# Optimization experiments

Measured on AMD Instinct MI355X. Metric: run time of the kernel, lower is better.

Reference implementation:

```python
import jax, jax.numpy as jnp
import numpy as np

NBINS = (128, 64, 32)
N_POINTS = 250_000
N_GENES = 5000
N_GENES_OI = 500
SUM_H = sum(NBINS)            # 224
SUM_W = sum(n - 1 for n in NBINS)  # 221


def _calculate_widths(unnormalized_widths):
    return jax.nn.softmax(unnormalized_widths, axis=-1)


def _calculate_bin_locations(widths):
    bl = jnp.cumsum(widths, axis=-1)
    bl = bl.at[..., -1].set(1.0)
    pad = [(0, 0)] * (bl.ndim - 1) + [(1, 0)]
    return jnp.pad(bl, pad)


def _calculate_heights(unnormalized_heights, widths):
    e = jnp.exp(unnormalized_heights)
    # trapezoid-rule area so pdf integrates to 1
    area = jnp.sum(0.5 * (e[..., :-1] + e[..., 1:]) * widths, axis=-1, keepdims=True)
    return e / area


def _calculate_bin_left_cdf(heights, widths):
    cdf = jnp.cumsum(0.5 * (heights[..., :-1] + heights[..., 1:]) * widths, axis=-1)
    cdf = cdf.at[..., -1].set(1.0)
    pad = [(0, 0)] * (cdf.ndim - 1) + [(1, 0)]
    return jnp.pad(cdf, pad)


def _quadratic_spline(x, widths, heights, bin_left_cdf, bin_locations):
    # all per-point: widths [N,nb], heights [N,nb+1], cdf/locations [N,nb+1]
    nb = widths.shape[-1]
    bin_idx = jnp.clip(jnp.sum(x[:, None] >= bin_locations, axis=-1) - 1, 0, nb - 1)

    def take(a, i):
        return jnp.take_along_axis(a, i[:, None], axis=-1)[:, 0]

    in_bl = take(bin_locations, bin_idx)
    in_cdf = take(bin_left_cdf, bin_idx)
    h_left = take(heights, bin_idx)
    h_right = take(heights, bin_idx + 1)
    w = take(widths, bin_idx)

    a = 0.5 * (h_right - h_left) * w
    b = h_left * w
    alpha = (x - in_bl) / w
    out = a * alpha * alpha + b * alpha + in_cdf
    logabsdet = jnp.log(alpha * (h_right - h_left) + h_left)
    return jnp.clip(out, 0.0, 1.0), logabsdet


def setup_inputs() -> dict:
    key = jax.random.key(0)
    k1, k2, k3, k4, k5, k6 = jax.random.split(key, 6)
    return {
        "x": jax.random.uniform(k1, (N_POINTS,), dtype=jnp.float32),
        "delta": jax.random.normal(k2, (N_POINTS, SUM_H), dtype=jnp.float32),
        "heights_weight": jax.random.normal(k3, (N_GENES, SUM_H), dtype=jnp.float32),
        "widths_weight": jax.random.normal(k4, (N_GENES, SUM_W), dtype=jnp.float32),
        "genes_oi": jax.random.randint(k5, (N_GENES_OI,), 0, N_GENES, dtype=jnp.int32),
        "local_gene_ix": jax.random.randint(k6, (N_POINTS,), 0, N_GENES_OI, dtype=jnp.int32),
    }


def reference(x, delta, heights_weight, widths_weight, genes_oi, local_gene_ix):
    # sparse embedding gather for the genes in the minibatch
    uh_all = heights_weight[genes_oi]   # [G_oi, sum_h]
    uw_all = widths_weight[genes_oi]    # [G_oi, sum_w]

    outputs = x
    logabsdet = jnp.zeros_like(x)
    h_off = 0
    w_off = 0
    d_off = 0
    for n in NBINS:
        uw = uw_all[:, w_off:w_off + (n - 1)]          # [G_oi, n-1]
        uh = uh_all[:, h_off:h_off + n]                # [G_oi, n]
        dh = delta[:, d_off:d_off + n]                 # [N, n]

        widths_g = _calculate_widths(uw)               # [G_oi, n-1]
        bin_loc_g = _calculate_bin_locations(widths_g) # [G_oi, n]

        widths = widths_g[local_gene_ix]               # [N, n-1]
        bin_locations = bin_loc_g[local_gene_ix]       # [N, n]
        uh_p = uh[local_gene_ix] + dh                  # [N, n]
        heights = _calculate_heights(uh_p, widths)     # [N, n]
        bin_left_cdf = _calculate_bin_left_cdf(heights, widths)  # [N, n]

        outputs, lad = _quadratic_spline(outputs, widths, heights, bin_left_cdf, bin_locations)
        logabsdet = logabsdet + lad

        h_off += n
        w_off += n - 1
        d_off += n
    return outputs, logabsdet
```

## Files before the change

kernel.cpp:

```cpp
#include <hip/hip_runtime.h>
#include <math.h>

#define SUM_H 224
#define SUM_W 221
#define ROWP  224

__global__ __launch_bounds__(64) void gene_tables_kernel(
    const float* __restrict__ heights_weight,
    const float* __restrict__ widths_weight,
    const int*   __restrict__ genes_oi,
    float* __restrict__ uh_t,
    float* __restrict__ w_t,
    float* __restrict__ bl_t,
    int n_genes)
{
    int g = blockIdx.x;
    if (g >= n_genes) return;
    int gi = genes_oi[g];
    int l  = threadIdx.x;

    {
        const float* src = heights_weight + (size_t)gi * SUM_H;
        float*       dst = uh_t + (size_t)g * ROWP;
        for (int j = l; j < SUM_H; j += 64) dst[j] = src[j];
    }

    const float* wsrc  = widths_weight + (size_t)gi * SUM_W;
    float*       wdst  = w_t  + (size_t)g * ROWP;
    float*       bldst = bl_t + (size_t)g * ROWP;

    const int ns[3]   = {128, 64, 32};
    const int woff[3] = {0, 127, 190};
    const int toff[3] = {0, 128, 192};

    for (int lev = 0; lev < 3; lev++) {
        int m  = ns[lev] - 1;
        int j0 = 2 * l, j1 = 2 * l + 1;
        float u0 = (j0 < m) ? wsrc[woff[lev] + j0] : -1e30f;
        float u1 = (j1 < m) ? wsrc[woff[lev] + j1] : -1e30f;
        float mx = fmaxf(u0, u1);
        #pragma unroll
        for (int msk = 32; msk >= 1; msk >>= 1)
            mx = fmaxf(mx, __shfl_xor(mx, msk, 64));
        float e0 = (j0 < m) ? __expf(u0 - mx) : 0.f;
        float e1 = (j1 < m) ? __expf(u1 - mx) : 0.f;
        float local = e0 + e1;
        float incl  = local;
        #pragma unroll
        for (int off = 1; off < 64; off <<= 1) {
            float t = __shfl_up(incl, off, 64);
            if (l >= off) incl += t;
        }
        float total = __shfl(incl, 63, 64);
        float inv   = 1.0f / total;
        float excl  = incl - local;
        if (j0 < m) wdst[toff[lev] + j0] = e0 * inv;
        if (j1 < m) wdst[toff[lev] + j1] = e1 * inv;
        float c0 = (excl + e0) * inv;
        float c1 = (excl + e0 + e1) * inv;
        if (j0 <= m - 2) bldst[toff[lev] + j0 + 1] = c0;
        if (j1 <= m - 2) bldst[toff[lev] + j1 + 1] = c1;
        if (l == 0) {
            bldst[toff[lev]]     = 0.0f;
            bldst[toff[lev] + m] = 1.0f;
        }
    }
}

template<int N>
__device__ inline void level_step(
    const float* __restrict__ dh,
    const float* __restrict__ uh,
    const float* __restrict__ bl,
    const float* __restrict__ wt,
    int e, float& x, float& lad)
{
    constexpr int NCH = (N + 63) / 64;
    constexpr int ACT = (N >= 64) ? 16 : (N / 4);

    float s[NCH][4];
    int cnt = 0;
    #pragma unroll
    for (int ch = 0; ch < NCH; ch++) {
        int c = ch * 64 + 4 * e;
        bool act = (e < ACT);
        if (act) {
            float4 dh4 = *reinterpret_cast<const float4*>(dh + c);
            float4 uh4 = *reinterpret_cast<const float4*>(uh + c);
            float4 bl4 = *reinterpret_cast<const float4*>(bl + c);
            float4 w4  = *reinterpret_cast<const float4*>(wt + c);
            bool hx = (c + 4) <= (N - 1);
            float dhx = hx ? dh[c + 4] : 0.f;
            float uhx = hx ? uh[c + 4] : 0.f;
            float E0 = __expf(uh4.x + dh4.x);
            float E1 = __expf(uh4.y + dh4.y);
            float E2 = __expf(uh4.z + dh4.z);
            float E3 = __expf(uh4.w + dh4.w);
            float E4 = __expf(uhx + dhx);
            cnt += (x >= bl4.x) + (x >= bl4.y) + (x >= bl4.z) + (x >= bl4.w);
            s[ch][0] = 0.5f * (E0 + E1) * w4.x;
            s[ch][1] = 0.5f * (E1 + E2) * w4.y;
            s[ch][2] = 0.5f * (E2 + E3) * w4.z;
            s[ch][3] = ((c + 3) <= (N - 2)) ? 0.5f * (E3 + E4) * w4.w : 0.f;
        } else {
            s[ch][0] = s[ch][1] = s[ch][2] = s[ch][3] = 0.f;
        }
    }

    #pragma unroll
    for (int msk = 8; msk >= 1; msk >>= 1)
        cnt += __shfl_xor(cnt, msk, 16);
    int idx = cnt - 1;
    if (idx > N - 2) idx = N - 2;

    float area = 0.f, part = 0.f;
    #pragma unroll
    for (int ch = 0; ch < NCH; ch++) {
        int c = ch * 64 + 4 * e;
        #pragma unroll
        for (int k = 0; k < 4; k++) {
            area += s[ch][k];
            part += ((c + k) < idx) ? s[ch][k] : 0.f;
        }
    }
    #pragma unroll
    for (int msk = 8; msk >= 1; msk >>= 1) {
        area += __shfl_xor(area, msk, 16);
        part += __shfl_xor(part, msk, 16);
    }

    float in_bl = bl[idx];
    float w     = wt[idx];
    float El    = __expf(uh[idx]     + dh[idx]);
    float Er    = __expf(uh[idx + 1] + dh[idx + 1]);

    float inv   = 1.0f / area;
    float hl    = El * inv;
    float hr    = Er * inv;
    float icdf  = part * inv;
    float alpha = (x - in_bl) / w;
    float dhh   = hr - hl;
    float out   = (0.5f * dhh * w) * alpha * alpha + (hl * w) * alpha + icdf;
    lad += __logf(alpha * dhh + hl);
    x = fminf(fmaxf(out, 0.f), 1.f);
}

__global__ __launch_bounds__(256) void spline_kernel(
    const float* __restrict__ x_in,
    const float* __restrict__ delta,
    const int*   __restrict__ lgx,
    const float* __restrict__ uh_t,
    const float* __restrict__ w_t,
    const float* __restrict__ bl_t,
    float* __restrict__ out,
    float* __restrict__ lad_out,
    int n_points)
{
    int tid = blockIdx.x * blockDim.x + threadIdx.x;
    int p = tid >> 4;
    int e = tid & 15;
    if (p >= n_points) return;

    int   g   = lgx[p];
    float x   = x_in[p];
    float lad = 0.f;

    const float* dh = delta + (size_t)p * SUM_H;
    const float* uh = uh_t + (size_t)g * ROWP;
    const float* bl = bl_t + (size_t)g * ROWP;
    const float* wt = w_t  + (size_t)g * ROWP;

    level_step<128>(dh,       uh,       bl,       wt,       e, x, lad);
    level_step<64> (dh + 128, uh + 128, bl + 128, wt + 128, e, x, lad);
    level_step<32> (dh + 192, uh + 192, bl + 192, wt + 192, e, x, lad);

    if (e == 0) {
        out[p]     = x;
        lad_out[p] = lad;
    }
}

extern "C" void kernel_launch(void* const* d_in, const int* in_sizes, int n_in,
                              void* d_out, int out_size, void* d_ws, size_t ws_size,
                              hipStream_t stream)
{
    const float* x        = (const float*)d_in[0];
    const float* delta    = (const float*)d_in[1];
    const float* hw       = (const float*)d_in[2];
    const float* ww       = (const float*)d_in[3];
    const int*   genes_oi = (const int*)  d_in[4];
    const int*   lgx      = (const int*)  d_in[5];

    int n_points   = in_sizes[0];
    int n_genes_oi = in_sizes[4];

    float* uh_t = (float*)d_ws;
    float* w_t  = uh_t + (size_t)n_genes_oi * ROWP;
    float* bl_t = w_t  + (size_t)n_genes_oi * ROWP;

    hipLaunchKernelGGL(gene_tables_kernel, dim3(n_genes_oi), dim3(64), 0, stream,
                       hw, ww, genes_oi, uh_t, w_t, bl_t, n_genes_oi);

    const int threads = 256;
    const int ppb     = threads / 16;
    const int blocks  = (n_points + ppb - 1) / ppb;
    hipLaunchKernelGGL(spline_kernel, dim3(blocks), dim3(threads), 0, stream,
                       x, delta, lgx, uh_t, w_t, bl_t,
                       (float*)d_out, (float*)d_out + n_points, n_points);
}
```

Baseline: 377.5 us.

## Prefetch all three spline levels into registers and select bins via shuffles

The spline kernel now loads the delta, height, bin-location and half-width data for all three levels at the start. Exps and areas are computed from registers, and each level's bin is selected with a register select followed by a shuffle from the owning lane, replacing the dependent global reloads that followed the bin search. Height weights are read straight from the gene table through genes_oi, which removes the copy in the table kernel. The 0.5 factor is folded into the stored widths and the trailing entries are zero-padded. This exposes more memory parallelism and removes serialized loads, at the cost of higher register pressure.

```diff
diff --git a/kernel.cpp b/kernel.cpp
--- a/kernel.cpp
+++ b/kernel.cpp
@@ -6,11 +6,9 @@
 #define ROWP  224
 
 __global__ __launch_bounds__(64) void gene_tables_kernel(
-    const float* __restrict__ heights_weight,
     const float* __restrict__ widths_weight,
     const int*   __restrict__ genes_oi,
-    float* __restrict__ uh_t,
-    float* __restrict__ w_t,
+    float* __restrict__ wh_t,
     float* __restrict__ bl_t,
     int n_genes)
 {
@@ -19,14 +17,8 @@
     int gi = genes_oi[g];
     int l  = threadIdx.x;
 
-    {
-        const float* src = heights_weight + (size_t)gi * SUM_H;
-        float*       dst = uh_t + (size_t)g * ROWP;
-        for (int j = l; j < SUM_H; j += 64) dst[j] = src[j];
-    }
-
     const float* wsrc  = widths_weight + (size_t)gi * SUM_W;
-    float*       wdst  = w_t  + (size_t)g * ROWP;
+    float*       wdst  = wh_t + (size_t)g * ROWP;
     float*       bldst = bl_t + (size_t)g * ROWP;
 
     const int ns[3]   = {128, 64, 32};
@@ -54,8 +46,8 @@
         float total = __shfl(incl, 63, 64);
         float inv   = 1.0f / total;
         float excl  = incl - local;
-        if (j0 < m) wdst[toff[lev] + j0] = e0 * inv;
-        if (j1 < m) wdst[toff[lev] + j1] = e1 * inv;
+        if (j0 < m) wdst[toff[lev] + j0] = 0.5f * e0 * inv;
+        if (j1 < m) wdst[toff[lev] + j1] = 0.5f * e1 * inv;
         float c0 = (excl + e0) * inv;
         float c1 = (excl + e0 + e1) * inv;
         if (j0 <= m - 2) bldst[toff[lev] + j0 + 1] = c0;
@@ -65,92 +57,120 @@
             bldst[toff[lev] + m] = 1.0f;
         }
     }
-}
-
-template<int N>
-__device__ inline void level_step(
-    const float* __restrict__ dh,
-    const float* __restrict__ uh,
-    const float* __restrict__ bl,
-    const float* __restrict__ wt,
-    int e, float& x, float& lad)
-{
-    constexpr int NCH = (N + 63) / 64;
-    constexpr int ACT = (N >= 64) ? 16 : (N / 4);
-
-    float s[NCH][4];
-    int cnt = 0;
-    #pragma unroll
-    for (int ch = 0; ch < NCH; ch++) {
-        int c = ch * 64 + 4 * e;
-        bool act = (e < ACT);
-        if (act) {
-            float4 dh4 = *reinterpret_cast<const float4*>(dh + c);
-            float4 uh4 = *reinterpret_cast<const float4*>(uh + c);
-            float4 bl4 = *reinterpret_cast<const float4*>(bl + c);
-            float4 w4  = *reinterpret_cast<const float4*>(wt + c);
-            bool hx = (c + 4) <= (N - 1);
-            float dhx = hx ? dh[c + 4] : 0.f;
-            float uhx = hx ? uh[c + 4] : 0.f;
-            float E0 = __expf(uh4.x + dh4.x);
-            float E1 = __expf(uh4.y + dh4.y);
-            float E2 = __expf(uh4.z + dh4.z);
-            float E3 = __expf(uh4.w + dh4.w);
-            float E4 = __expf(uhx + dhx);
-            cnt += (x >= bl4.x) + (x >= bl4.y) + (x >= bl4.z) + (x >= bl4.w);
-            s[ch][0] = 0.5f * (E0 + E1) * w4.x;
-            s[ch][1] = 0.5f * (E1 + E2) * w4.y;
-            s[ch][2] = 0.5f * (E2 + E3) * w4.z;
-            s[ch][3] = ((c + 3) <= (N - 2)) ? 0.5f * (E3 + E4) * w4.w : 0.f;
-        } else {
-            s[ch][0] = s[ch][1] = s[ch][2] = s[ch][3] = 0.f;
-        }
-    }
-
-    #pragma unroll
-    for (int msk = 8; msk >= 1; msk >>= 1)
-        cnt += __shfl_xor(cnt, msk, 16);
+    if (l == 0) { wdst[127] = 0.f; wdst[191] = 0.f; wdst[223] = 0.f; }
+}
+
+template<int K>
+struct Lvl {
+    float E[K + 1];
+    float bl[K];
+    float wh[K];
+    float s[K];
+    float bln;
+    float area;
+};
+
+template<int K>
+__device__ __forceinline__ void lvl_fetch(const float* __restrict__ dh,
+                                          const float* __restrict__ uh,
+                                          const float* __restrict__ blp,
+                                          const float* __restrict__ whp,
+                                          int e, Lvl<K>& L)
+{
+    const int j = K * e;
+    if constexpr (K == 8) {
+        *(float4*)&L.E[0]  = *(const float4*)(uh  + j);
+        *(float4*)&L.E[4]  = *(const float4*)(uh  + j + 4);
+        *(float4*)&L.s[0]  = *(const float4*)(dh  + j);
+        *(float4*)&L.s[4]  = *(const float4*)(dh  + j + 4);
+        *(float4*)&L.bl[0] = *(const float4*)(blp + j);
+        *(float4*)&L.bl[4] = *(const float4*)(blp + j + 4);
+        *(float4*)&L.wh[0] = *(const float4*)(whp + j);
+        *(float4*)&L.wh[4] = *(const float4*)(whp + j + 4);
+    } else if constexpr (K == 4) {
+        *(float4*)&L.E[0]  = *(const float4*)(uh  + j);
+        *(float4*)&L.s[0]  = *(const float4*)(dh  + j);
+        *(float4*)&L.bl[0] = *(const float4*)(blp + j);
+        *(float4*)&L.wh[0] = *(const float4*)(whp + j);
+    } else {
+        *(float2*)&L.E[0]  = *(const float2*)(uh  + j);
+        *(float2*)&L.s[0]  = *(const float2*)(dh  + j);
+        *(float2*)&L.bl[0] = *(const float2*)(blp + j);
+        *(float2*)&L.wh[0] = *(const float2*)(whp + j);
+    }
+}
+
+template<int K>
+__device__ __forceinline__ void lvl_finish(int e, Lvl<K>& L)
+{
+    #pragma unroll
+    for (int k = 0; k < K; k++) L.E[k] = __expf(L.E[k] + L.s[k]);
+    L.E[K] = __shfl_down(L.E[0], 1, 16);
+    L.bln  = __shfl_down(L.bl[0], 1, 16);
+    #pragma unroll
+    for (int k = 0; k < K; k++) L.s[k] = (L.E[k] + L.E[k + 1]) * L.wh[k];
+    if (e == 15) L.s[K - 1] = 0.f;
+    float a = 0.f;
+    #pragma unroll
+    for (int k = 0; k < K; k++) a += L.s[k];
+    #pragma unroll
+    for (int m = 8; m >= 1; m >>= 1) a += __shfl_xor(a, m, 16);
+    L.area = a;
+}
+
+template<int N, int K>
+__device__ __forceinline__ void lvl_apply(const Lvl<K>& L, float& x, float& lad)
+{
+    constexpr int LOGK = (K == 8) ? 3 : (K == 4) ? 2 : 1;
+    int   cnt  = 0;
+    float part = 0.f;
+    #pragma unroll
+    for (int k = 0; k < K; k++) cnt += (x >= L.bl[k]) ? 1 : 0;
+    #pragma unroll
+    for (int k = 0; k < K - 1; k++) part += (x >= L.bl[k + 1]) ? L.s[k] : 0.f;
+    part += (x >= L.bln) ? L.s[K - 1] : 0.f;
+
+    #pragma unroll
+    for (int m = 8; m >= 1; m >>= 1) {
+        cnt  += __shfl_xor(cnt,  m, 16);
+        part += __shfl_xor(part, m, 16);
+    }
     int idx = cnt - 1;
     if (idx > N - 2) idx = N - 2;
-
-    float area = 0.f, part = 0.f;
-    #pragma unroll
-    for (int ch = 0; ch < NCH; ch++) {
-        int c = ch * 64 + 4 * e;
-        #pragma unroll
-        for (int k = 0; k < 4; k++) {
-            area += s[ch][k];
-            part += ((c + k) < idx) ? s[ch][k] : 0.f;
-        }
-    }
-    #pragma unroll
-    for (int msk = 8; msk >= 1; msk >>= 1) {
-        area += __shfl_xor(area, msk, 16);
-        part += __shfl_xor(part, msk, 16);
-    }
-
-    float in_bl = bl[idx];
-    float w     = wt[idx];
-    float El    = __expf(uh[idx]     + dh[idx]);
-    float Er    = __expf(uh[idx + 1] + dh[idx + 1]);
-
-    float inv   = 1.0f / area;
-    float hl    = El * inv;
-    float hr    = Er * inv;
-    float icdf  = part * inv;
-    float alpha = (x - in_bl) / w;
-    float dhh   = hr - hl;
-    float out   = (0.5f * dhh * w) * alpha * alpha + (hl * w) * alpha + icdf;
-    lad += __logf(alpha * dhh + hl);
-    x = fminf(fmaxf(out, 0.f), 1.f);
+    const int owner = idx >> LOGK;
+    const int slot  = idx & (K - 1);
+
+    float sE = L.E[0], sE1 = L.E[1], sB = L.bl[0], sW = L.wh[0];
+    #pragma unroll
+    for (int jj = 1; jj < K; jj++) {
+        bool m = (slot == jj);
+        sE  = m ? L.E[jj]     : sE;
+        sE1 = m ? L.E[jj + 1] : sE1;
+        sB  = m ? L.bl[jj]    : sB;
+        sW  = m ? L.wh[jj]    : sW;
+    }
+    float hlr = __shfl(sE,  owner, 16);
+    float hrr = __shfl(sE1, owner, 16);
+    float inb = __shfl(sB,  owner, 16);
+    float whs = __shfl(sW,  owner, 16);
+
+    float inva  = __builtin_amdgcn_rcpf(L.area);
+    float hl    = hlr * inva;
+    float dhh   = (hrr - hlr) * inva;
+    float icdf  = part * inva;
+    float alpha = (x - inb) * __builtin_amdgcn_rcpf(whs + whs);
+    float outv  = fmaf(fmaf(whs, dhh * alpha, (hl + hl) * whs), alpha, icdf);
+    lad += __logf(fmaf(alpha, dhh, hl));
+    x = __builtin_amdgcn_fmed3f(outv, 0.0f, 1.0f);
 }
 
 __global__ __launch_bounds__(256) void spline_kernel(
     const float* __restrict__ x_in,
     const float* __restrict__ delta,
     const int*   __restrict__ lgx,
-    const float* __restrict__ uh_t,
-    const float* __restrict__ w_t,
+    const int*   __restrict__ genes_oi,
+    const float* __restrict__ heights_weight,
+    const float* __restrict__ wh_t,
     const float* __restrict__ bl_t,
     float* __restrict__ out,
     float* __restrict__ lad_out,
@@ -161,18 +181,26 @@
     int e = tid & 15;
     if (p >= n_points) return;
 
-    int   g   = lgx[p];
+    int g  = lgx[p];
+    int gi = genes_oi[g];
+    const float* dh = delta          + (size_t)p  * SUM_H;
+    const float* uh = heights_weight + (size_t)gi * SUM_H;
+    const float* bl = bl_t + (size_t)g * ROWP;
+    const float* wh = wh_t + (size_t)g * ROWP;
+
+    Lvl<8> L0; Lvl<4> L1; Lvl<2> L2;
+    lvl_fetch<8>(dh,       uh,       bl,       wh,       e, L0);
+    lvl_fetch<4>(dh + 128, uh + 128, bl + 128, wh + 128, e, L1);
+    lvl_fetch<2>(dh + 192, uh + 192, bl + 192, wh + 192, e, L2);
     float x   = x_in[p];
     float lad = 0.f;
-
-    const float* dh = delta + (size_t)p * SUM_H;
-    const float* uh = uh_t + (size_t)g * ROWP;
-    const float* bl = bl_t + (size_t)g * ROWP;
-    const float* wt = w_t  + (size_t)g * ROWP;
-
-    level_step<128>(dh,       uh,       bl,       wt,       e, x, lad);
-    level_step<64> (dh + 128, uh + 128, bl + 128, wt + 128, e, x, lad);
-    level_step<32> (dh + 192, uh + 192, bl + 192, wt + 192, e, x, lad);
+    lvl_finish<8>(e, L0);
+    lvl_finish<4>(e, L1);
+    lvl_finish<2>(e, L2);
+
+    lvl_apply<128, 8>(L0, x, lad);
+    lvl_apply<64,  4>(L1, x, lad);
+    lvl_apply<32,  2>(L2, x, lad);
 
     if (e == 0) {
         out[p]     = x;
@@ -194,17 +222,16 @@
     int n_points   = in_sizes[0];
     int n_genes_oi = in_sizes[4];
 
-    float* uh_t = (float*)d_ws;
-    float* w_t  = uh_t + (size_t)n_genes_oi * ROWP;
-    float* bl_t = w_t  + (size_t)n_genes_oi * ROWP;
+    float* wh_t = (float*)d_ws;
+    float* bl_t = wh_t + (size_t)n_genes_oi * ROWP;
 
     hipLaunchKernelGGL(gene_tables_kernel, dim3(n_genes_oi), dim3(64), 0, stream,
-                       hw, ww, genes_oi, uh_t, w_t, bl_t, n_genes_oi);
+                       ww, genes_oi, wh_t, bl_t, n_genes_oi);
 
     const int threads = 256;
     const int ppb     = threads / 16;
     const int blocks  = (n_points + ppb - 1) / ppb;
     hipLaunchKernelGGL(spline_kernel, dim3(blocks), dim3(threads), 0, stream,
-                       x, delta, lgx, uh_t, w_t, bl_t,
+                       x, delta, lgx, genes_oi, hw, wh_t, bl_t,
                        (float*)d_out, (float*)d_out + n_points, n_points);
 }
```

Result: faster. 351.4 us (-6.9%).

## Switch to one thread per point with precomputed interleaved float4 gene tables

Applied to the files above, without the earlier changes.

Replaces the 16-lanes-per-point spline with one thread per point that walks all bins sequentially. The gene kernel now precomputes per-bin edges and width-scaled exp(height) halves into a gene-interleaved float4 table, so the hot loop only needs exp(delta) and FMAs. The log is deferred to a single log of a running product, with a constant added for the normalisation. This removes cross-lane shuffles and redundant exp/gather work. In exchange, per-thread delta rows become strided uncoalesced loads, register pressure rises, and the product-of-terms log changes numerics.

```diff
diff --git a/kernel.cpp b/kernel.cpp
--- a/kernel.cpp
+++ b/kernel.cpp
@@ -3,35 +3,27 @@
 
 #define SUM_H 224
 #define SUM_W 221
-#define ROWP  224
+
 
 __global__ __launch_bounds__(64) void gene_tables_kernel(
     const float* __restrict__ heights_weight,
     const float* __restrict__ widths_weight,
     const int*   __restrict__ genes_oi,
-    float* __restrict__ uh_t,
-    float* __restrict__ w_t,
-    float* __restrict__ bl_t,
-    int n_genes)
+    float4* __restrict__ tbl,
+    int ng)
 {
     int g = blockIdx.x;
-    if (g >= n_genes) return;
+    if (g >= ng) return;
     int gi = genes_oi[g];
     int l  = threadIdx.x;
 
-    {
-        const float* src = heights_weight + (size_t)gi * SUM_H;
-        float*       dst = uh_t + (size_t)g * ROWP;
-        for (int j = l; j < SUM_H; j += 64) dst[j] = src[j];
-    }
-
-    const float* wsrc  = widths_weight + (size_t)gi * SUM_W;
-    float*       wdst  = w_t  + (size_t)g * ROWP;
-    float*       bldst = bl_t + (size_t)g * ROWP;
+    const float* wsrc = widths_weight  + (size_t)gi * SUM_W;
+    const float* hsrc = heights_weight + (size_t)gi * SUM_H;
 
     const int ns[3]   = {128, 64, 32};
     const int woff[3] = {0, 127, 190};
-    const int toff[3] = {0, 128, 192};
+    const int hoff[3] = {0, 128, 192};
+    const int kb[3]   = {0, 127, 190};
 
     for (int lev = 0; lev < 3; lev++) {
         int m  = ns[lev] - 1;
@@ -54,129 +46,107 @@
         float total = __shfl(incl, 63, 64);
         float inv   = 1.0f / total;
         float excl  = incl - local;
-        if (j0 < m) wdst[toff[lev] + j0] = e0 * inv;
-        if (j1 < m) wdst[toff[lev] + j1] = e1 * inv;
-        float c0 = (excl + e0) * inv;
-        float c1 = (excl + e0 + e1) * inv;
-        if (j0 <= m - 2) bldst[toff[lev] + j0 + 1] = c0;
-        if (j1 <= m - 2) bldst[toff[lev] + j1 + 1] = c1;
-        if (l == 0) {
-            bldst[toff[lev]]     = 0.0f;
-            bldst[toff[lev] + m] = 1.0f;
-        }
+        float edge0 = excl * inv;
+        float edge1 = (excl + e0) * inv;
+        float w0    = e0 * inv;
+        float w1    = e1 * inv;
+        float h0 = (j0 < m) ? __expf(hsrc[hoff[lev] + j0])     : 0.f;
+        float h1 = (j0 < m) ? __expf(hsrc[hoff[lev] + j0 + 1]) : 0.f;
+        float h2 = (j1 < m) ? __expf(hsrc[hoff[lev] + j1 + 1]) : 0.f;
+        if (j0 < m) tbl[(size_t)(kb[lev] + j0) * ng + g] =
+            make_float4(edge0, 0.5f * w0 * h0, 0.5f * w0 * h1, 0.f);
+        if (j1 < m) tbl[(size_t)(kb[lev] + j1) * ng + g] =
+            make_float4(edge1, 0.5f * w1 * h1, 0.5f * w1 * h2, 0.f);
     }
 }
 
 template<int N>
-__device__ inline void level_step(
-    const float* __restrict__ dh,
-    const float* __restrict__ uh,
-    const float* __restrict__ bl,
-    const float* __restrict__ wt,
-    int e, float& x, float& lad)
+__device__ __forceinline__ void walk(const float* __restrict__ dhl,
+                                     const float4* __restrict__ tp,
+                                     int ng, float& x, float& prod)
 {
-    constexpr int NCH = (N + 63) / 64;
-    constexpr int ACT = (N >= 64) ? 16 : (N / 4);
+    constexpr int M  = N - 1;
+    constexpr int NC = N / 4;
 
-    float s[NCH][4];
-    int cnt = 0;
+    float4 q[8];
     #pragma unroll
-    for (int ch = 0; ch < NCH; ch++) {
-        int c = ch * 64 + 4 * e;
-        bool act = (e < ACT);
-        if (act) {
-            float4 dh4 = *reinterpret_cast<const float4*>(dh + c);
-            float4 uh4 = *reinterpret_cast<const float4*>(uh + c);
-            float4 bl4 = *reinterpret_cast<const float4*>(bl + c);
-            float4 w4  = *reinterpret_cast<const float4*>(wt + c);
-            bool hx = (c + 4) <= (N - 1);
-            float dhx = hx ? dh[c + 4] : 0.f;
-            float uhx = hx ? uh[c + 4] : 0.f;
-            float E0 = __expf(uh4.x + dh4.x);
-            float E1 = __expf(uh4.y + dh4.y);
-            float E2 = __expf(uh4.z + dh4.z);
-            float E3 = __expf(uh4.w + dh4.w);
-            float E4 = __expf(uhx + dhx);
-            cnt += (x >= bl4.x) + (x >= bl4.y) + (x >= bl4.z) + (x >= bl4.w);
-            s[ch][0] = 0.5f * (E0 + E1) * w4.x;
-            s[ch][1] = 0.5f * (E1 + E2) * w4.y;
-            s[ch][2] = 0.5f * (E2 + E3) * w4.z;
-            s[ch][3] = ((c + 3) <= (N - 2)) ? 0.5f * (E3 + E4) * w4.w : 0.f;
-        } else {
-            s[ch][0] = s[ch][1] = s[ch][2] = s[ch][3] = 0.f;
+    for (int i = 0; i < 8; i++) q[i] = *(const float4*)(dhl + 4 * i);
+    float4 tq[2][4];
+    #pragma unroll
+    for (int t = 0; t < 4; t++) tq[0][t] = tp[(size_t)t * ng];
+
+    float ed    = __expf(q[0].x);
+    float area  = 0.f, part = 0.f, sprev = 0.f;
+    float inb   = 0.f, b1 = 1.0f, Pk = 0.f, Sk = 0.f;
+
+    #pragma unroll
+    for (int ci = 0; ci < NC; ci++) {
+        float4 cur = q[ci & 7];
+        float dv[4];
+        dv[0] = cur.y; dv[1] = cur.z; dv[2] = cur.w;
+        dv[3] = (4 * ci + 4 <= M) ? q[(ci + 1) & 7].x : 0.f;
+        if (ci + 8 < NC) q[ci & 7] = *(const float4*)(dhl + 4 * (ci + 8));
+        #pragma unroll
+        for (int t = 0; t < 4; t++) {
+            int sl = 4 * (ci + 1) + t;
+            if (sl < M) tq[(ci + 1) & 1][t] = tp[(size_t)sl * ng];
+        }
+        #pragma unroll
+        for (int t = 0; t < 4; t++) {
+            int j = 4 * ci + t;
+            if (j < M) {
+                float4 tt  = tq[ci & 1][t];
+                float  ed1 = __expf(dv[t]);
+                float  P   = tt.y * ed;
+                float  s   = fmaf(tt.z, ed1, P);
+                area += s;
+                bool   c   = (x >= tt.x);
+                part += c ? sprev : 0.f;
+                inb   = c ? tt.x : inb;
+                Pk    = c ? P    : Pk;
+                Sk    = c ? s    : Sk;
+                b1    = c ? b1   : fminf(b1, tt.x);
+                sprev = s;
+                ed    = ed1;
+            }
         }
     }
-
-    #pragma unroll
-    for (int msk = 8; msk >= 1; msk >>= 1)
-        cnt += __shfl_xor(cnt, msk, 16);
-    int idx = cnt - 1;
-    if (idx > N - 2) idx = N - 2;
-
-    float area = 0.f, part = 0.f;
-    #pragma unroll
-    for (int ch = 0; ch < NCH; ch++) {
-        int c = ch * 64 + 4 * e;
-        #pragma unroll
-        for (int k = 0; k < 4; k++) {
-            area += s[ch][k];
-            part += ((c + k) < idx) ? s[ch][k] : 0.f;
-        }
-    }
-    #pragma unroll
-    for (int msk = 8; msk >= 1; msk >>= 1) {
-        area += __shfl_xor(area, msk, 16);
-        part += __shfl_xor(part, msk, 16);
-    }
-
-    float in_bl = bl[idx];
-    float w     = wt[idx];
-    float El    = __expf(uh[idx]     + dh[idx]);
-    float Er    = __expf(uh[idx + 1] + dh[idx + 1]);
-
-    float inv   = 1.0f / area;
-    float hl    = El * inv;
-    float hr    = Er * inv;
-    float icdf  = part * inv;
-    float alpha = (x - in_bl) / w;
-    float dhh   = hr - hl;
-    float out   = (0.5f * dhh * w) * alpha * alpha + (hl * w) * alpha + icdf;
-    lad += __logf(alpha * dhh + hl);
-    x = fminf(fmaxf(out, 0.f), 1.f);
+    float w     = b1 - inb;
+    float rw    = __builtin_amdgcn_rcpf(w);
+    float inva  = __builtin_amdgcn_rcpf(area);
+    float dEh   = fmaf(-2.f, Pk, Sk);
+    float alpha = (x - inb) * rw;
+    float poly  = fmaf(fmaf(dEh, alpha, Pk + Pk), alpha, part);
+    x = __builtin_amdgcn_fmed3f(poly * inva, 0.f, 1.f);
+    prod *= fmaf(alpha, dEh, Pk) * (rw * inva);
 }
 
 __global__ __launch_bounds__(256) void spline_kernel(
     const float* __restrict__ x_in,
     const float* __restrict__ delta,
     const int*   __restrict__ lgx,
-    const float* __restrict__ uh_t,
-    const float* __restrict__ w_t,
-    const float* __restrict__ bl_t,
+    const float4* __restrict__ tbl,
+    int ng,
     float* __restrict__ out,
     float* __restrict__ lad_out,
     int n_points)
 {
-    int tid = blockIdx.x * blockDim.x + threadIdx.x;
-    int p = tid >> 4;
-    int e = tid & 15;
-    if (p >= n_points) return;
+    int p  = blockIdx.x * 256 + threadIdx.x;
+    int pc = (p < n_points) ? p : (n_points - 1);
 
-    int   g   = lgx[p];
-    float x   = x_in[p];
-    float lad = 0.f;
+    float x = x_in[pc];
+    int   g = lgx[pc];
+    const float*  dh = delta + (size_t)pc * SUM_H;
+    const float4* tg = tbl + g;
 
-    const float* dh = delta + (size_t)p * SUM_H;
-    const float* uh = uh_t + (size_t)g * ROWP;
-    const float* bl = bl_t + (size_t)g * ROWP;
-    const float* wt = w_t  + (size_t)g * ROWP;
+    float prod = 1.f;
+    walk<128>(dh,       tg,                    ng, x, prod);
+    walk<64> (dh + 128, tg + (size_t)127 * ng, ng, x, prod);
+    walk<32> (dh + 192, tg + (size_t)190 * ng, ng, x, prod);
 
-    level_step<128>(dh,       uh,       bl,       wt,       e, x, lad);
-    level_step<64> (dh + 128, uh + 128, bl + 128, wt + 128, e, x, lad);
-    level_step<32> (dh + 192, uh + 192, bl + 192, wt + 192, e, x, lad);
-
-    if (e == 0) {
+    if (p < n_points) {
         out[p]     = x;
-        lad_out[p] = lad;
+        lad_out[p] = __logf(prod) + 2.0794415416798357f;
     }
 }
 
@@ -194,17 +164,13 @@
     int n_points   = in_sizes[0];
     int n_genes_oi = in_sizes[4];
 
-    float* uh_t = (float*)d_ws;
-    float* w_t  = uh_t + (size_t)n_genes_oi * ROWP;
-    float* bl_t = w_t  + (size_t)n_genes_oi * ROWP;
+    float4* tbl = (float4*)d_ws;
 
     hipLaunchKernelGGL(gene_tables_kernel, dim3(n_genes_oi), dim3(64), 0, stream,
-                       hw, ww, genes_oi, uh_t, w_t, bl_t, n_genes_oi);
+                       hw, ww, genes_oi, tbl, n_genes_oi);
 
-    const int threads = 256;
-    const int ppb     = threads / 16;
-    const int blocks  = (n_points + ppb - 1) / ppb;
-    hipLaunchKernelGGL(spline_kernel, dim3(blocks), dim3(threads), 0, stream,
-                       x, delta, lgx, uh_t, w_t, bl_t,
+    const int blocks = (n_points + 255) / 256;
+    hipLaunchKernelGGL(spline_kernel, dim3(blocks), dim3(256), 0, stream,
+                       x, delta, lgx, tbl, n_genes_oi,
                        (float*)d_out, (float*)d_out + n_points, n_points);
 }
```

After: 431.9 us. 14.4% more time.
